# Kernel optimization log

Measured on AMD Instinct MI355X. Metric: run time of the kernel, lower is better.

The kernel has to match this reference:

```python
import jax, jax.numpy as jnp
from jax import lax
import numpy as np

N, K, L, H, LAT = 2048, 8, 64, 512, 128
NHPN, NNUC = 4, 5

def setup_inputs() -> dict:
    key = jax.random.key(0)
    ks = jax.random.split(key, 16)
    def w(k, shape):
        return (jax.random.normal(k, shape, jnp.float32) / jnp.sqrt(shape[-1])).astype(jnp.float32)
    return {
        'hpn_idx': jax.random.randint(ks[0], (N,), 0, NHPN),
        'nuc_idx': jax.random.randint(ks[1], (N, L), 0, NNUC),
        'h_nei': jax.random.normal(ks[2], (N, K, H), jnp.float32),
        'graph_latent': jax.random.normal(ks[3], (N, LAT), jnp.float32),
        'Wz_mp': w(ks[4], (H, H + NHPN)), 'bz_mp': jnp.zeros((H,), jnp.float32),
        'Wr_mp': w(ks[5], (H, NHPN)), 'br_mp': jnp.zeros((H,), jnp.float32),
        'Ur_mp': w(ks[6], (H, H)),
        'Wh_mp': w(ks[7], (H, H + NHPN)), 'bh_mp': jnp.zeros((H,), jnp.float32),
        'Wz_nuc': w(ks[8], (H, H + NNUC)), 'bz_nuc': jnp.zeros((H,), jnp.float32),
        'Wr_nuc': w(ks[9], (H, H + NNUC)), 'br_nuc': jnp.zeros((H,), jnp.float32),
        'Wh_nuc': w(ks[10], (H, H + NNUC)), 'bh_nuc': jnp.zeros((H,), jnp.float32),
        'W_hpn_nl': w(ks[11], (H, H)), 'b_hpn_nl': jnp.zeros((H,), jnp.float32),
        'W_hpn': w(ks[12], (NHPN, H)), 'b_hpn': jnp.zeros((NHPN,), jnp.float32),
        'W_nuc_nl': w(ks[13], (H, H + LAT)), 'b_nuc_nl': jnp.zeros((H,), jnp.float32),
        'W_nuc': w(ks[14], (NNUC, H)), 'b_nuc': jnp.zeros((NNUC,), jnp.float32),
        'W_topo_nl': w(ks[15], (H, H)), 'b_topo_nl': jnp.zeros((H,), jnp.float32),
        'W_topo': w(jax.random.fold_in(key, 99), (1, H)), 'b_topo': jnp.zeros((1,), jnp.float32),
    }

def _graph_gru(x, h_nei, Wz, bz, Wr, br, Ur, Wh, bh):
    # x: [N, 4] hpn one-hot; h_nei: [N, K, H] padded incoming messages
    sum_h = h_nei.sum(axis=1)
    z = jax.nn.sigmoid(jnp.concatenate([x, sum_h], axis=1) @ Wz.T + bz)
    r = jax.nn.sigmoid((x @ Wr.T + br)[:, None, :] + jnp.einsum('nkh,oh->nko', h_nei, Ur))
    sum_gated = (r * h_nei).sum(axis=1)
    pre_h = jnp.tanh(jnp.concatenate([x, sum_gated], axis=1) @ Wh.T + bh)
    return (1.0 - z) * sum_h + z * pre_h

def reference(hpn_idx, nuc_idx, h_nei, graph_latent, Wz_mp, bz_mp, Wr_mp, br_mp, Ur_mp, Wh_mp, bh_mp,
              Wz_nuc, bz_nuc, Wr_nuc, br_nuc, Wh_nuc, bh_nuc,
              W_hpn_nl, b_hpn_nl, W_hpn, b_hpn, W_nuc_nl, b_nuc_nl, W_nuc, b_nuc,
              W_topo_nl, b_topo_nl, W_topo, b_topo):
    dt = h_nei.dtype
    hpn_oh = jax.nn.one_hot(hpn_idx, NHPN, dtype=dt)
    # GraphGRU message aggregation
    msg = _graph_gru(hpn_oh, h_nei, Wz_mp, bz_mp, Wr_mp, br_mp, Ur_mp, Wh_mp, bh_mp)  # [N, H]
    # teacher-forced per-nucleotide GRU
    seq = jax.nn.one_hot(nuc_idx, NNUC, dtype=dt)  # [N, L, 5]
    def step(h, xt):
        zi = jnp.concatenate([xt, h], axis=1)
        z = jax.nn.sigmoid(zi @ Wz_nuc.T + bz_nuc)
        r = jax.nn.sigmoid(zi @ Wr_nuc.T + br_nuc)
        hi = jnp.concatenate([xt, r * h], axis=1)
        pre = jnp.tanh(hi @ Wh_nuc.T + bh_nuc)
        nh = (1.0 - z) * h + z * pre
        return nh, nh
    new_h, hs = lax.scan(step, msg, jnp.swapaxes(seq, 0, 1))  # hs: [L, N, H]
    hs = jnp.swapaxes(hs, 0, 1)  # [N, L, H]
    # nuc head: cat([hidden, graph_latent]) -> relu -> logits, without materializing the concat
    hid_part = jnp.einsum('nlh,oh->nlo', hs, W_nuc_nl[:, :H])
    lat_part = graph_latent @ W_nuc_nl[:, H:].T  # [N, H]
    nuc_hidden = jax.nn.relu(hid_part + lat_part[:, None, :] + b_nuc_nl)
    nuc_logits = jnp.einsum('nlh,oh->nlo', nuc_hidden, W_nuc) + b_nuc  # [N, L, 5]
    # hpn head on new message hidden
    hpn_logits = jax.nn.relu(new_h @ W_hpn_nl.T + b_hpn_nl) @ W_hpn.T + b_hpn  # [N, 4]
    # stop/topology head on GraphGRU output
    stop_logits = jax.nn.relu(msg @ W_topo_nl.T + b_topo_nl) @ W_topo.T + b_topo  # [N, 1]
    return jnp.concatenate([new_h.ravel(), hpn_logits.ravel(), nuc_logits.ravel(), stop_logits.ravel()])
```

## Files before the change

kernel.cpp:

```cpp
#include <hip/hip_runtime.h>
#include <math.h>

#define NROWS 2048
#define KNEI  8
#define LSEQ  64
#define HD    512
#define HD4   128
#define LATD  128
#define NHPN  4
#define NNUC  5

typedef __attribute__((ext_vector_type(8))) short s8b;
typedef __attribute__((ext_vector_type(4))) short s4b;
typedef __attribute__((ext_vector_type(4))) float f4;

#define MFMA16(a,b,c) __builtin_amdgcn_mfma_f32_16x16x32_bf16(a,b,c,0,0,0)

__device__ __forceinline__ f4 f4zero(){ f4 z; z[0]=0.f; z[1]=0.f; z[2]=0.f; z[3]=0.f; return z; }
__device__ __forceinline__ float sigf(float x){ return __fdividef(1.0f, 1.0f + __expf(-x)); }
__device__ __forceinline__ float tanhf_fast(float x){
  float e = __expf(-2.0f*fabsf(x));
  float t = __fdividef(1.0f - e, 1.0f + e);
  return x >= 0.f ? t : -t;
}
__device__ __forceinline__ unsigned short f2bf(float x){
  union{float f; unsigned u;} v; v.f = x;
  unsigned r = (v.u + 0x7FFFu + ((v.u>>16)&1u)) >> 16;
  return (unsigned short)r;
}
__device__ __forceinline__ void add4(float4& a, float4 b){ a.x+=b.x; a.y+=b.y; a.z+=b.z; a.w+=b.w; }

__device__ __forceinline__ void dma16(const short* g, const short* l){
  __builtin_amdgcn_global_load_lds(
      (const __attribute__((address_space(1))) void*)(unsigned long long)g,
      (__attribute__((address_space(3))) void*)(unsigned long long)l,
      16, 0, 0);
}


__global__ void transpose_w(const float* __restrict__ src, float* __restrict__ dst,
                            int src_cols, int col_off, int nh){
  int idx = blockIdx.x*256 + threadIdx.x;
  if (idx >= nh*HD) return;
  int h = idx / HD, o = idx - h*HD;
  dst[idx] = src[o*src_cols + col_off + h];
}

__global__ void fragprep_k(const float* __restrict__ W, short* __restrict__ dst,
                           int src_cols, int col_off){
  int idx = blockIdx.x*256 + threadIdx.x;
  if (idx >= HD*HD) return;
  int j = idx&7, l = (idx>>3)&63, tile = idx>>9;
  int kc = tile&15, ot = tile>>4;
  int row = ot*16 + (l&15), k = kc*32 + (l>>4)*8 + j;
  dst[idx] = (short)f2bf(W[(size_t)row*src_cols + col_off + k]);
}

__global__ void wxbprep2_k(const float* __restrict__ W, const float* __restrict__ b,
                           float* __restrict__ dst, int src_cols, int nc){
  int idx = blockIdx.x*256 + threadIdx.x;
  if (idx >= nc*HD) return;
  int c = idx/HD, n = idx - c*HD;
  dst[idx] = W[(size_t)n*src_cols + c] + b[n];
}

__global__ __launch_bounds__(512) void latp_k(const float* __restrict__ gl, const float* __restrict__ wtlat,
                     const float* __restrict__ bnl, float* __restrict__ latp){
  __shared__ float gls[16][LATD];
  int b = blockIdx.x, t = threadIdx.x;
  for (int i=t;i<16*LATD;i+=512) gls[i/LATD][i%LATD] = gl[(size_t)(b*16)*LATD + i];
  __syncthreads();
  float acc[16];
  float bv = bnl[t];
  #pragma unroll
  for (int r=0;r<16;++r) acc[r]=bv;
  for (int q=0;q<LATD;++q){
    float wv = wtlat[(size_t)q*HD + t];
    #pragma unroll
    for (int r=0;r<16;++r) acc[r] = fmaf(gls[r][q], wv, acc[r]);
  }
  #pragma unroll
  for (int r=0;r<16;++r) latp[(size_t)(b*16+r)*HD + t] = acc[r];
}

__global__ void sumcast_k(const float* __restrict__ h_nei,
                          float* __restrict__ sumhF, short* __restrict__ sumhB){
  int idx = blockIdx.x*512 + threadIdx.x;
  int n = idx >> 7, c4 = idx & 127;
  const float4* hn4 = (const float4*)h_nei;
  size_t base = (size_t)n*KNEI*HD4 + c4;
  float4 s = hn4[base];
  #pragma unroll
  for (int k=1;k<KNEI;++k) add4(s, hn4[base + (size_t)k*HD4]);
  ((float4*)sumhF)[(size_t)n*HD4 + c4] = s;
  s4b p;
  p[0]=(short)f2bf(s.x); p[1]=(short)f2bf(s.y); p[2]=(short)f2bf(s.z); p[3]=(short)f2bf(s.w);
  ((s4b*)sumhB)[(size_t)n*HD4 + c4] = p;
}

__global__ __launch_bounds__(512) void ggru_gemm_k(
    int mode,
    const short* __restrict__ frag,
    const short* __restrict__ A,
    const int* __restrict__ hpn_idx,
    const float* __restrict__ bias_tab,
    const float* __restrict__ sumhF, const float* __restrict__ zF_in,
    const float* __restrict__ w_topo,
    float* __restrict__ zF_out,
    float* __restrict__ hF, short* __restrict__ hB,
    float* __restrict__ topo_p)
{
  __shared__ __align__(16) short stage[16][4096];
  __shared__ int codes_s[32];
  const int tt = threadIdx.x, l = tt&63, w = tt>>6, lm = l&15, g = l>>4;
  const int rt = blockIdx.x, row0 = rt*32, cg = blockIdx.y;
  if (tt<32) codes_s[tt] = hpn_idx[row0+tt];
  const int mt = w>>2, ntp = w&3;
  const short* gsrc = frag + ((size_t)(cg*8 + w)*16)*512 + (size_t)l*8;
  #pragma unroll
  for (int kc=0;kc<8;++kc) dma16(gsrc + (size_t)kc*512, &stage[kc][w*512 + l*8]);
  s8b af[16];
  {
    const s8b* arow = (const s8b*)(A + (size_t)(row0 + mt*16 + lm)*HD);
    #pragma unroll
    for (int kc=0;kc<16;++kc) af[kc] = arow[kc*4 + g];
  }
  asm volatile("s_waitcnt vmcnt(0)" ::: "memory");
  __syncthreads();
  #pragma unroll
  for (int kc=8;kc<16;++kc) dma16(gsrc + (size_t)kc*512, &stage[kc][w*512 + l*8]);
  f4 acc[2]; acc[0]=f4zero(); acc[1]=f4zero();
  #pragma unroll
  for (int kc=0;kc<8;++kc){
    #pragma unroll
    for (int i2=0;i2<2;++i2){
      s8b b = ((const s8b*)&stage[kc][(ntp*2+i2)*512])[l];
      acc[i2] = MFMA16(af[kc], b, acc[i2]);
    }
  }
  asm volatile("s_waitcnt vmcnt(0)" ::: "memory");
  __syncthreads();
  #pragma unroll
  for (int kc=8;kc<16;++kc){
    #pragma unroll
    for (int i2=0;i2<2;++i2){
      s8b b = ((const s8b*)&stage[kc][(ntp*2+i2)*512])[l];
      acc[i2] = MFMA16(af[kc], b, acc[i2]);
    }
  }
  if (mode==0){
    #pragma unroll
    for (int i2=0;i2<2;++i2){
      const int col = cg*128 + (ntp*2+i2)*16 + lm;
      #pragma unroll
      for (int q=0;q<4;++q){
        const int r = mt*16 + g*4 + q;
        zF_out[(size_t)(row0+r)*HD + col] = sigf(acc[i2][q] + bias_tab[codes_s[r]*HD + col]);
      }
    }
  } else if (mode==1){
    #pragma unroll
    for (int i2=0;i2<2;++i2){
      const int col = cg*128 + (ntp*2+i2)*16 + lm;
      #pragma unroll
      for (int q=0;q<4;++q){
        const int r = mt*16 + g*4 + q;
        const size_t idx = (size_t)(row0+r)*HD + col;
        float pre = tanhf_fast(acc[i2][q] + bias_tab[codes_s[r]*HD + col]);
        float zv = zF_in[idx];
        float m = (1.f - zv)*sumhF[idx] + zv*pre;
        hF[idx] = m;
        hB[idx] = (short)f2bf(m);
      }
    }
  } else {
    float p[4];
    #pragma unroll
    for (int q=0;q<4;++q) p[q]=0.f;
    #pragma unroll
    for (int i2=0;i2<2;++i2){
      const int col = cg*128 + (ntp*2+i2)*16 + lm;
      float wv = w_topo[col];
      float bnl = bias_tab[col];
      #pragma unroll
      for (int q=0;q<4;++q){
        float hid = fmaxf(acc[i2][q] + bnl, 0.f);
        p[q] = fmaf(hid, wv, p[q]);
      }
    }
    #pragma unroll
    for (int s=1;s<16;s<<=1)
      #pragma unroll
      for (int q=0;q<4;++q) p[q] += __shfl_xor(p[q], s);
    if (lm==0){
      #pragma unroll
      for (int q=0;q<4;++q)
        topo_p[(size_t)(cg*4+ntp)*NROWS + row0 + mt*16 + g*4 + q] = p[q];
    }
  }
}

__global__ __launch_bounds__(512) void ggru_r_k(
    const short* __restrict__ fUr,
    const float* __restrict__ h_nei,
    const int* __restrict__ hpn_idx,
    const float* __restrict__ wxbr_mp,
    short* __restrict__ sgB)
{
  __shared__ __align__(16) short stage[16][4096];
  __shared__ float gat[32][128];
  __shared__ int codes_s[32];
  const int tt = threadIdx.x, l = tt&63, w = tt>>6, lm = l&15, g = l>>4;
  const int rt = blockIdx.x, row0 = rt*32, cg = blockIdx.y;
  if (tt<32) codes_s[tt] = hpn_idx[(row0+tt)>>3];
  const int mt = w>>2, ntp = w&3;
  const short* gsrc = fUr + ((size_t)(cg*8 + w)*16)*512 + (size_t)l*8;
  #pragma unroll
  for (int kc=0;kc<8;++kc) dma16(gsrc + (size_t)kc*512, &stage[kc][w*512 + l*8]);
  s8b af[16];
  {
    const float* hrow = h_nei + (size_t)(row0 + mt*16 + lm)*HD;
    #pragma unroll
    for (int kc=0;kc<16;++kc){
      float4 v0 = *(const float4*)&hrow[kc*32 + g*8];
      float4 v1 = *(const float4*)&hrow[kc*32 + g*8 + 4];
      s8b a;
      a[0]=(short)f2bf(v0.x); a[1]=(short)f2bf(v0.y); a[2]=(short)f2bf(v0.z); a[3]=(short)f2bf(v0.w);
      a[4]=(short)f2bf(v1.x); a[5]=(short)f2bf(v1.y); a[6]=(short)f2bf(v1.z); a[7]=(short)f2bf(v1.w);
      af[kc] = a;
    }
  }
  asm volatile("s_waitcnt vmcnt(0)" ::: "memory");
  __syncthreads();
  #pragma unroll
  for (int kc=8;kc<16;++kc) dma16(gsrc + (size_t)kc*512, &stage[kc][w*512 + l*8]);
  f4 acc[2]; acc[0]=f4zero(); acc[1]=f4zero();
  #pragma unroll
  for (int kc=0;kc<8;++kc){
    #pragma unroll
    for (int i2=0;i2<2;++i2){
      s8b b = ((const s8b*)&stage[kc][(ntp*2+i2)*512])[l];
      acc[i2] = MFMA16(af[kc], b, acc[i2]);
    }
  }
  asm volatile("s_waitcnt vmcnt(0)" ::: "memory");
  __syncthreads();
  #pragma unroll
  for (int kc=8;kc<16;++kc){
    #pragma unroll
    for (int i2=0;i2<2;++i2){
      s8b b = ((const s8b*)&stage[kc][(ntp*2+i2)*512])[l];
      acc[i2] = MFMA16(af[kc], b, acc[i2]);
    }
  }
  #pragma unroll
  for (int i2=0;i2<2;++i2){
    const int lc = (ntp*2+i2)*16 + lm;
    const int col = cg*128 + lc;
    #pragma unroll
    for (int q=0;q<4;++q){
      const int r = mt*16 + g*4 + q;
      float rv = sigf(acc[i2][q] + wxbr_mp[codes_s[r]*HD + col]);
      gat[r][lc] = rv * h_nei[(size_t)(row0+r)*HD + col];
    }
  }
  __syncthreads();
  {
    int j = tt >> 7, c = tt & 127;
    float s = 0.f;
    #pragma unroll
    for (int k=0;k<8;++k) s += gat[j*8+k][c];
    sgB[(size_t)(rt*4 + j)*HD + cg*128 + c] = (short)f2bf(s);
  }
}

__global__ __launch_bounds__(512) void zrnuc_k(
    int t, const int* __restrict__ nuc_idx,
    const short* __restrict__ fz, const short* __restrict__ fr, const short* __restrict__ fnuc,
    const short* __restrict__ hB, const float* __restrict__ hF,
    const float* __restrict__ wxbz, const float* __restrict__ wxbr,
    const float* __restrict__ latp, const float* __restrict__ w_nuc,
    float* __restrict__ zF, short* __restrict__ ghB, float* __restrict__ nucp)
{
  const int cg = blockIdx.y;
  const int mat = cg>>2;
  if (t==0 && mat==2) return;
  __shared__ __align__(16) short stage[16][4096];
  __shared__ int codes_s[64];
  const int tt = threadIdx.x, l = tt&63, w = tt>>6, lm = l&15, g = l>>4;
  const int rt = blockIdx.x, row0 = rt*64;
  const short* frag = (mat==0)?fz:((mat==1)?fr:fnuc);
  const int otb = (cg&3)*8;
  if (tt<64) codes_s[tt] = nuc_idx[(size_t)(row0+tt)*LSEQ + t];
  const int mt = w>>1, nh2 = w&1;
  const short* gsrc = frag + ((size_t)(otb + w)*16)*512 + (size_t)l*8;
  #pragma unroll
  for (int kc=0;kc<8;++kc) dma16(gsrc + (size_t)kc*512, &stage[kc][w*512 + l*8]);
  s8b af[16];
  {
    const s8b* hrow = (const s8b*)(hB + (size_t)(row0 + mt*16 + lm)*HD);
    #pragma unroll
    for (int kc=0;kc<16;++kc) af[kc] = hrow[kc*4 + g];
  }
  asm volatile("s_waitcnt vmcnt(0)" ::: "memory");
  __syncthreads();
  #pragma unroll
  for (int kc=8;kc<16;++kc) dma16(gsrc + (size_t)kc*512, &stage[kc][w*512 + l*8]);
  f4 acc[4];
  #pragma unroll
  for (int i=0;i<4;++i) acc[i]=f4zero();
  #pragma unroll
  for (int kc=0;kc<8;++kc){
    #pragma unroll
    for (int i=0;i<4;++i){
      s8b b = ((const s8b*)&stage[kc][(nh2*4+i)*512])[l];
      acc[i] = MFMA16(af[kc], b, acc[i]);
    }
  }
  asm volatile("s_waitcnt vmcnt(0)" ::: "memory");
  __syncthreads();
  #pragma unroll
  for (int kc=8;kc<16;++kc){
    #pragma unroll
    for (int i=0;i<4;++i){
      s8b b = ((const s8b*)&stage[kc][(nh2*4+i)*512])[l];
      acc[i] = MFMA16(af[kc], b, acc[i]);
    }
  }
  const int colb = (cg&3)*128;
  if (mat==0){
    #pragma unroll
    for (int i=0;i<4;++i){
      const int col = colb + (nh2*4+i)*16 + lm;
      #pragma unroll
      for (int q=0;q<4;++q){
        const int r = mt*16 + g*4 + q;
        float zv = sigf(acc[i][q] + wxbz[codes_s[r]*HD + col]);
        zF[(size_t)(row0+r)*HD + col] = zv;
      }
    }
  } else if (mat==1){
    #pragma unroll
    for (int i=0;i<4;++i){
      const int col = colb + (nh2*4+i)*16 + lm;
      #pragma unroll
      for (int q=0;q<4;++q){
        const int r = mt*16 + g*4 + q;
        float rv = sigf(acc[i][q] + wxbr[codes_s[r]*HD + col]);
        ghB[(size_t)(row0+r)*HD + col] = (short)f2bf(rv * hF[(size_t)(row0+r)*HD + col]);
      }
    }
  } else {
    float p[4][NNUC];
    #pragma unroll
    for (int q=0;q<4;++q)
      #pragma unroll
      for (int j=0;j<NNUC;++j) p[q][j]=0.f;
    #pragma unroll
    for (int i=0;i<4;++i){
      const int col = colb + (nh2*4+i)*16 + lm;
      #pragma unroll
      for (int q=0;q<4;++q){
        const int r = mt*16 + g*4 + q;
        float hid = fmaxf(acc[i][q] + latp[(size_t)(row0+r)*HD + col], 0.f);
        #pragma unroll
        for (int j=0;j<NNUC;++j) p[q][j] = fmaf(hid, w_nuc[(size_t)j*HD + col], p[q][j]);
      }
    }
    #pragma unroll
    for (int s=1;s<16;s<<=1)
      #pragma unroll
      for (int q=0;q<4;++q)
        #pragma unroll
        for (int j=0;j<NNUC;++j) p[q][j] += __shfl_xor(p[q][j], s);
    if (lm==0){
      const int slab = (cg&3)*2 + nh2;
      #pragma unroll
      for (int q=0;q<4;++q){
        const int row = row0 + mt*16 + g*4 + q;
        #pragma unroll
        for (int j=0;j<NNUC;++j)
          nucp[((size_t)slab*NROWS + row)*NNUC + j] = p[q][j];
      }
    }
  }
}

__global__ __launch_bounds__(512) void cand_k(
    int t, const int* __restrict__ nuc_idx,
    const short* __restrict__ fh,
    const short* __restrict__ ghB,
    const float* __restrict__ wxbh,
    const float* __restrict__ zF, float* __restrict__ hF, short* __restrict__ hB,
    const float* __restrict__ nucp, const float* __restrict__ b_nuc,
    float* __restrict__ out_nuc)
{
  __shared__ __align__(16) short stage[16][4096];
  __shared__ int codes_s[32];
  const int tt = threadIdx.x, l = tt&63, w = tt>>6, lm = l&15, g = l>>4;
  const int rt = blockIdx.x, row0 = rt*32, cg = blockIdx.y;
  if (tt<32) codes_s[tt] = nuc_idx[(size_t)(row0+tt)*LSEQ + t];
  const int mt = w>>2, ntp = w&3;
  const short* gsrc = fh + ((size_t)(cg*8 + w)*16)*512 + (size_t)l*8;
  #pragma unroll
  for (int kc=0;kc<8;++kc) dma16(gsrc + (size_t)kc*512, &stage[kc][w*512 + l*8]);
  s8b af[16];
  {
    const s8b* grow = (const s8b*)(ghB + (size_t)(row0 + mt*16 + lm)*HD);
    #pragma unroll
    for (int kc=0;kc<16;++kc) af[kc] = grow[kc*4 + g];
  }
  asm volatile("s_waitcnt vmcnt(0)" ::: "memory");
  __syncthreads();
  #pragma unroll
  for (int kc=8;kc<16;++kc) dma16(gsrc + (size_t)kc*512, &stage[kc][w*512 + l*8]);
  f4 acc[2]; acc[0]=f4zero(); acc[1]=f4zero();
  #pragma unroll
  for (int kc=0;kc<8;++kc){
    #pragma unroll
    for (int i2=0;i2<2;++i2){
      s8b b = ((const s8b*)&stage[kc][(ntp*2+i2)*512])[l];
      acc[i2] = MFMA16(af[kc], b, acc[i2]);
    }
  }
  asm volatile("s_waitcnt vmcnt(0)" ::: "memory");
  __syncthreads();
  #pragma unroll
  for (int kc=8;kc<16;++kc){
    #pragma unroll
    for (int i2=0;i2<2;++i2){
      s8b b = ((const s8b*)&stage[kc][(ntp*2+i2)*512])[l];
      acc[i2] = MFMA16(af[kc], b, acc[i2]);
    }
  }
  #pragma unroll
  for (int i2=0;i2<2;++i2){
    const int col = cg*128 + (ntp*2+i2)*16 + lm;
    #pragma unroll
    for (int q=0;q<4;++q){
      const int r = mt*16 + g*4 + q;
      const size_t idx = (size_t)(row0+r)*HD + col;
      float pre = tanhf_fast(acc[i2][q] + wxbh[codes_s[r]*HD + col]);
      float zv = zF[idx];
      float hn = (1.f - zv)*hF[idx] + zv*pre;
      hF[idx] = hn;
      hB[idx] = (short)f2bf(hn);
    }
  }
  if (t > 0 && cg == 0 && tt < 32*NNUC){
    int rr = tt/NNUC, j = tt - rr*NNUC;
    int row = row0 + rr;
    float s2 = b_nuc[j];
    #pragma unroll
    for (int s8=0;s8<8;++s8) s2 += nucp[((size_t)s8*NROWS + row)*NNUC + j];
    out_nuc[((size_t)row*LSEQ + (t-1))*NNUC + j] = s2;
  }
}

__global__ __launch_bounds__(512) void heads_k(
    const short* __restrict__ fnuc, const short* __restrict__ fhpn,
    const short* __restrict__ hB,
    const float* __restrict__ latp, const float* __restrict__ w_nuc,
    const float* __restrict__ b_hpn_nl, const float* __restrict__ w_hpn,
    float* __restrict__ nucpH, float* __restrict__ hpnp)
{
  __shared__ __align__(16) short stage[16][4096];
  const int tt = threadIdx.x, l = tt&63, w = tt>>6, lm = l&15, g = l>>4;
  const int rt = blockIdx.x, row0 = rt*32, cg = blockIdx.y;
  const int mat = cg>>2;
  const short* frag = mat ? fhpn : fnuc;
  const int mt = w>>2, ntp = w&3;
  const short* gsrc = frag + ((size_t)((cg&3)*8 + w)*16)*512 + (size_t)l*8;
  #pragma unroll
  for (int kc=0;kc<8;++kc) dma16(gsrc + (size_t)kc*512, &stage[kc][w*512 + l*8]);
  s8b af[16];
  {
    const s8b* hrow = (const s8b*)(hB + (size_t)(row0 + mt*16 + lm)*HD);
    #pragma unroll
    for (int kc=0;kc<16;++kc) af[kc] = hrow[kc*4 + g];
  }
  asm volatile("s_waitcnt vmcnt(0)" ::: "memory");
  __syncthreads();
  #pragma unroll
  for (int kc=8;kc<16;++kc) dma16(gsrc + (size_t)kc*512, &stage[kc][w*512 + l*8]);
  f4 acc[2]; acc[0]=f4zero(); acc[1]=f4zero();
  #pragma unroll
  for (int kc=0;kc<8;++kc){
    #pragma unroll
    for (int i2=0;i2<2;++i2){
      s8b b = ((const s8b*)&stage[kc][(ntp*2+i2)*512])[l];
      acc[i2] = MFMA16(af[kc], b, acc[i2]);
    }
  }
  asm volatile("s_waitcnt vmcnt(0)" ::: "memory");
  __syncthreads();
  #pragma unroll
  for (int kc=8;kc<16;++kc){
    #pragma unroll
    for (int i2=0;i2<2;++i2){
      s8b b = ((const s8b*)&stage[kc][(ntp*2+i2)*512])[l];
      acc[i2] = MFMA16(af[kc], b, acc[i2]);
    }
  }
  const int slab = (cg&3)*4 + ntp;
  if (mat==0){
    float p[4][NNUC];
    #pragma unroll
    for (int q=0;q<4;++q)
      #pragma unroll
      for (int j=0;j<NNUC;++j) p[q][j]=0.f;
    #pragma unroll
    for (int i2=0;i2<2;++i2){
      const int col = (cg&3)*128 + (ntp*2+i2)*16 + lm;
      #pragma unroll
      for (int q=0;q<4;++q){
        const int r = mt*16 + g*4 + q;
        float hid = fmaxf(acc[i2][q] + latp[(size_t)(row0+r)*HD + col], 0.f);
        #pragma unroll
        for (int j=0;j<NNUC;++j) p[q][j] = fmaf(hid, w_nuc[(size_t)j*HD + col], p[q][j]);
      }
    }
    #pragma unroll
    for (int s=1;s<16;s<<=1)
      #pragma unroll
      for (int q=0;q<4;++q)
        #pragma unroll
        for (int j=0;j<NNUC;++j) p[q][j] += __shfl_xor(p[q][j], s);
    if (lm==0){
      #pragma unroll
      for (int q=0;q<4;++q){
        const int row = row0 + mt*16 + g*4 + q;
        #pragma unroll
        for (int j=0;j<NNUC;++j)
          nucpH[((size_t)slab*NROWS + row)*NNUC + j] = p[q][j];
      }
    }
  } else {
    float p[4][NHPN];
    #pragma unroll
    for (int q=0;q<4;++q)
      #pragma unroll
      for (int j=0;j<NHPN;++j) p[q][j]=0.f;
    #pragma unroll
    for (int i2=0;i2<2;++i2){
      const int col = (cg&3)*128 + (ntp*2+i2)*16 + lm;
      float bnl = b_hpn_nl[col];
      #pragma unroll
      for (int q=0;q<4;++q){
        float hid = fmaxf(acc[i2][q] + bnl, 0.f);
        #pragma unroll
        for (int j=0;j<NHPN;++j) p[q][j] = fmaf(hid, w_hpn[(size_t)j*HD + col], p[q][j]);
      }
    }
    #pragma unroll
    for (int s=1;s<16;s<<=1)
      #pragma unroll
      for (int q=0;q<4;++q)
        #pragma unroll
        for (int j=0;j<NHPN;++j) p[q][j] += __shfl_xor(p[q][j], s);
    if (lm==0){
      #pragma unroll
      for (int q=0;q<4;++q){
        const int row = row0 + mt*16 + g*4 + q;
        #pragma unroll
        for (int j=0;j<NHPN;++j)
          hpnp[((size_t)slab*NROWS + row)*NHPN + j] = p[q][j];
      }
    }
  }
}

__global__ void final_red_k(const float* __restrict__ nucpH, const float* __restrict__ hpnp,
    const float* __restrict__ topo_p,
    const float* __restrict__ b_nuc, const float* __restrict__ b_hpn, const float* __restrict__ b_topo,
    const float* __restrict__ hF,
    float* __restrict__ out_newh, float* __restrict__ out_hpn, float* __restrict__ out_nuc,
    float* __restrict__ out_stop)
{
  int gid = blockIdx.x*256 + threadIdx.x;
  if (gid < NROWS*NNUC){
    int n = gid/NNUC, j = gid - n*NNUC;
    float s = b_nuc[j];
    #pragma unroll
    for (int s8=0;s8<16;++s8) s += nucpH[((size_t)s8*NROWS + n)*NNUC + j];
    out_nuc[((size_t)n*LSEQ + 63)*NNUC + j] = s;
  } else if (gid < NROWS*NNUC + NROWS*NHPN){
    int g2 = gid - NROWS*NNUC;
    int n = g2/NHPN, j = g2 - n*NHPN;
    float s = b_hpn[j];
    #pragma unroll
    for (int s8=0;s8<16;++s8) s += hpnp[((size_t)s8*NROWS + n)*NHPN + j];
    out_hpn[(size_t)n*NHPN + j] = s;
  } else if (gid < NROWS*NNUC + NROWS*NHPN + NROWS){
    int n = gid - (NROWS*NNUC + NROWS*NHPN);
    float s = b_topo[0];
    #pragma unroll
    for (int s16=0;s16<16;++s16) s += topo_p[(size_t)s16*NROWS + n];
    out_stop[n] = s;
  }
  const float4* src = (const float4*)hF;
  float4* dst = (float4*)out_newh;
  for (int i = gid; i < NROWS*HD/4; i += 32768) dst[i] = src[i];
}

extern "C" void kernel_launch(void* const* d_in, const int* in_sizes, int n_in,
                              void* d_out, int out_size, void* d_ws, size_t ws_size,
                              hipStream_t stream_){
  (void)in_sizes; (void)n_in; (void)out_size; (void)ws_size;
  const int*   hpn_idx      = (const int*)d_in[0];
  const int*   nuc_idx      = (const int*)d_in[1];
  const float* h_nei        = (const float*)d_in[2];
  const float* graph_latent = (const float*)d_in[3];
  const float* Wz_mp=(const float*)d_in[4];  const float* bz_mp=(const float*)d_in[5];
  const float* Wr_mp=(const float*)d_in[6];  const float* br_mp=(const float*)d_in[7];
  const float* Ur_mp=(const float*)d_in[8];
  const float* Wh_mp=(const float*)d_in[9];  const float* bh_mp=(const float*)d_in[10];
  const float* Wz_nuc=(const float*)d_in[11]; const float* bz_nuc=(const float*)d_in[12];
  const float* Wr_nuc=(const float*)d_in[13]; const float* br_nuc=(const float*)d_in[14];
  const float* Wh_nuc=(const float*)d_in[15]; const float* bh_nuc=(const float*)d_in[16];
  const float* W_hpn_nl=(const float*)d_in[17]; const float* b_hpn_nl=(const float*)d_in[18];
  const float* W_hpn=(const float*)d_in[19];  const float* b_hpn=(const float*)d_in[20];
  const float* W_nuc_nl=(const float*)d_in[21]; const float* b_nuc_nl=(const float*)d_in[22];
  const float* W_nuc=(const float*)d_in[23];  const float* b_nuc=(const float*)d_in[24];
  const float* W_topo_nl=(const float*)d_in[25]; const float* b_topo_nl=(const float*)d_in[26];
  const float* W_topo=(const float*)d_in[27]; const float* b_topo=(const float*)d_in[28];

  float* ws = (float*)d_ws;
  size_t off = 0;
  auto take = [&](size_t nfl){ float* p = ws + off; off += nfl; return p; };
  float* wt_nl_lat = take((size_t)LATD*HD);
  short* fz    = (short*)take((size_t)HD*HD/2);
  short* fr    = (short*)take((size_t)HD*HD/2);
  short* fh    = (short*)take((size_t)HD*HD/2);
  short* fnuc  = (short*)take((size_t)HD*HD/2);
  short* fhpn  = (short*)take((size_t)HD*HD/2);
  short* fWzh  = (short*)take((size_t)HD*HD/2);
  short* fUr   = (short*)take((size_t)HD*HD/2);
  short* fWhh  = (short*)take((size_t)HD*HD/2);
  short* fWtopo= (short*)take((size_t)HD*HD/2);
  float* wxbz = take((size_t)NNUC*HD);
  float* wxbr = take((size_t)NNUC*HD);
  float* wxbh = take((size_t)NNUC*HD);
  float* wxbz_mp = take((size_t)NHPN*HD);
  float* wxbr_mp = take((size_t)NHPN*HD);
  float* wxbh_mp = take((size_t)NHPN*HD);
  float* latp = take((size_t)NROWS*HD);
  float* hF   = take((size_t)NROWS*HD);
  short* hB   = (short*)take((size_t)NROWS*HD/2);
  short* ghB  = (short*)take((size_t)NROWS*HD/2);
  float* zF   = take((size_t)NROWS*HD);
  float* sumhF = take((size_t)NROWS*HD);
  short* sumhB = (short*)take((size_t)NROWS*HD/2);
  short* sgB   = (short*)take((size_t)NROWS*HD/2);
  float* nucp = take((size_t)8*NROWS*NNUC);
  float* nucpH= take((size_t)16*NROWS*NNUC);
  float* hpnp = take((size_t)16*NROWS*NHPN);
  float* topo_p = take((size_t)16*NROWS);

  float* out       = (float*)d_out;
  float* out_newh  = out;
  float* out_hpn   = out + (size_t)NROWS*HD;
  float* out_nuc   = out_hpn + (size_t)NROWS*NHPN;
  float* out_stop  = out_nuc + (size_t)NROWS*LSEQ*NNUC;

  transpose_w<<<(LATD*HD+255)/256, 256, 0, stream_>>>(W_nuc_nl, wt_nl_lat, HD+LATD, HD, LATD);

  const int FB = (HD*HD+255)/256;
  fragprep_k<<<FB,256,0,stream_>>>(Wz_nuc,   fz,    HD+NNUC, NNUC);
  fragprep_k<<<FB,256,0,stream_>>>(Wr_nuc,   fr,    HD+NNUC, NNUC);
  fragprep_k<<<FB,256,0,stream_>>>(Wh_nuc,   fh,    HD+NNUC, NNUC);
  fragprep_k<<<FB,256,0,stream_>>>(W_nuc_nl, fnuc,  HD+LATD, 0);
  fragprep_k<<<FB,256,0,stream_>>>(W_hpn_nl, fhpn,  HD,      0);
  fragprep_k<<<FB,256,0,stream_>>>(Wz_mp,    fWzh,  HD+NHPN, NHPN);
  fragprep_k<<<FB,256,0,stream_>>>(Ur_mp,    fUr,   HD,      0);
  fragprep_k<<<FB,256,0,stream_>>>(Wh_mp,    fWhh,  HD+NHPN, NHPN);
  fragprep_k<<<FB,256,0,stream_>>>(W_topo_nl,fWtopo,HD,      0);

  const int WB = (NNUC*HD+255)/256;
  wxbprep2_k<<<WB,256,0,stream_>>>(Wz_nuc, bz_nuc, wxbz, HD+NNUC, NNUC);
  wxbprep2_k<<<WB,256,0,stream_>>>(Wr_nuc, br_nuc, wxbr, HD+NNUC, NNUC);
  wxbprep2_k<<<WB,256,0,stream_>>>(Wh_nuc, bh_nuc, wxbh, HD+NNUC, NNUC);
  const int WB2 = (NHPN*HD+255)/256;
  wxbprep2_k<<<WB2,256,0,stream_>>>(Wz_mp, bz_mp, wxbz_mp, HD+NHPN, NHPN);
  wxbprep2_k<<<WB2,256,0,stream_>>>(Wr_mp, br_mp, wxbr_mp, NHPN,    NHPN);
  wxbprep2_k<<<WB2,256,0,stream_>>>(Wh_mp, bh_mp, wxbh_mp, HD+NHPN, NHPN);

  latp_k<<<NROWS/16, 512, 0, stream_>>>(graph_latent, wt_nl_lat, b_nuc_nl, latp);

  sumcast_k<<<512, 512, 0, stream_>>>(h_nei, sumhF, sumhB);
  ggru_gemm_k<<<dim3(64,4), 512, 0, stream_>>>(
      0, fWzh, sumhB, hpn_idx, wxbz_mp, nullptr, nullptr, nullptr,
      zF, nullptr, nullptr, nullptr);
  ggru_r_k<<<dim3(512,4), 512, 0, stream_>>>(fUr, h_nei, hpn_idx, wxbr_mp, sgB);
  ggru_gemm_k<<<dim3(64,4), 512, 0, stream_>>>(
      1, fWhh, sgB, hpn_idx, wxbh_mp, sumhF, zF, nullptr,
      nullptr, hF, hB, nullptr);
  ggru_gemm_k<<<dim3(64,4), 512, 0, stream_>>>(
      2, fWtopo, hB, hpn_idx, b_topo_nl, nullptr, nullptr, W_topo,
      nullptr, nullptr, nullptr, topo_p);

  for (int t = 0; t < LSEQ; ++t){
    zrnuc_k<<<dim3(32,12), 512, 0, stream_>>>(
        t, nuc_idx, fz, fr, fnuc, hB, hF,
        wxbz, wxbr, latp, W_nuc, zF, ghB, nucp);
    cand_k<<<dim3(64,4), 512, 0, stream_>>>(
        t, nuc_idx, fh, ghB, wxbh, zF, hF, hB,
        nucp, b_nuc, out_nuc);
  }

  heads_k<<<dim3(64,8), 512, 0, stream_>>>(
      fnuc, fhpn, hB, latp, W_nuc, b_hpn_nl, W_hpn, nucpH, hpnp);
  final_red_k<<<128, 256, 0, stream_>>>(
      nucpH, hpnp, topo_p, b_nuc, b_hpn, b_topo, hF,
      out_newh, out_hpn, out_nuc, out_stop);
}
```

Before: 2.132 ms.

## Enlarge per-block row tiles and precast neighbor messages to bf16

```diff
diff --git a/kernel.cpp b/kernel.cpp
--- a/kernel.cpp
+++ b/kernel.cpp
@@ -28,6 +28,9 @@
   unsigned r = (v.u + 0x7FFFu + ((v.u>>16)&1u)) >> 16;
   return (unsigned short)r;
 }
+__device__ __forceinline__ float bf2f(unsigned short u){
+  union{unsigned x; float f;} v; v.x = ((unsigned)u)<<16; return v.f;
+}
 __device__ __forceinline__ void add4(float4& a, float4 b){ a.x+=b.x; a.y+=b.y; a.z+=b.z; a.w+=b.w; }
 
 __device__ __forceinline__ void dma16(const short* g, const short* l){
@@ -84,14 +87,21 @@
 }
 
 __global__ void sumcast_k(const float* __restrict__ h_nei,
-                          float* __restrict__ sumhF, short* __restrict__ sumhB){
+                          float* __restrict__ sumhF, short* __restrict__ sumhB,
+                          short* __restrict__ hnB){
   int idx = blockIdx.x*512 + threadIdx.x;
   int n = idx >> 7, c4 = idx & 127;
   const float4* hn4 = (const float4*)h_nei;
   size_t base = (size_t)n*KNEI*HD4 + c4;
-  float4 s = hn4[base];
-  #pragma unroll
-  for (int k=1;k<KNEI;++k) add4(s, hn4[base + (size_t)k*HD4]);
+  float4 s = make_float4(0.f,0.f,0.f,0.f);
+  #pragma unroll
+  for (int k=0;k<KNEI;++k){
+    float4 v = hn4[base + (size_t)k*HD4];
+    add4(s, v);
+    s4b pb;
+    pb[0]=(short)f2bf(v.x); pb[1]=(short)f2bf(v.y); pb[2]=(short)f2bf(v.z); pb[3]=(short)f2bf(v.w);
+    ((s4b*)hnB)[(size_t)(n*KNEI + k)*HD4 + c4] = pb;
+  }
   ((float4*)sumhF)[(size_t)n*HD4 + c4] = s;
   s4b p;
   p[0]=(short)f2bf(s.x); p[1]=(short)f2bf(s.y); p[2]=(short)f2bf(s.z); p[3]=(short)f2bf(s.w);
@@ -202,45 +212,38 @@
 
 __global__ __launch_bounds__(512) void ggru_r_k(
     const short* __restrict__ fUr,
-    const float* __restrict__ h_nei,
+    const short* __restrict__ hnB,
     const int* __restrict__ hpn_idx,
     const float* __restrict__ wxbr_mp,
     short* __restrict__ sgB)
 {
   __shared__ __align__(16) short stage[16][4096];
-  __shared__ float gat[32][128];
-  __shared__ int codes_s[32];
+  __shared__ int codes_s[16];
   const int tt = threadIdx.x, l = tt&63, w = tt>>6, lm = l&15, g = l>>4;
-  const int rt = blockIdx.x, row0 = rt*32, cg = blockIdx.y;
-  if (tt<32) codes_s[tt] = hpn_idx[(row0+tt)>>3];
-  const int mt = w>>2, ntp = w&3;
+  const int row0 = blockIdx.x*128, cg = blockIdx.y;
+  if (tt<16) codes_s[tt] = hpn_idx[(row0>>3) + tt];
   const short* gsrc = fUr + ((size_t)(cg*8 + w)*16)*512 + (size_t)l*8;
   #pragma unroll
   for (int kc=0;kc<8;++kc) dma16(gsrc + (size_t)kc*512, &stage[kc][w*512 + l*8]);
   s8b af[16];
   {
-    const float* hrow = h_nei + (size_t)(row0 + mt*16 + lm)*HD;
-    #pragma unroll
-    for (int kc=0;kc<16;++kc){
-      float4 v0 = *(const float4*)&hrow[kc*32 + g*8];
-      float4 v1 = *(const float4*)&hrow[kc*32 + g*8 + 4];
-      s8b a;
-      a[0]=(short)f2bf(v0.x); a[1]=(short)f2bf(v0.y); a[2]=(short)f2bf(v0.z); a[3]=(short)f2bf(v0.w);
-      a[4]=(short)f2bf(v1.x); a[5]=(short)f2bf(v1.y); a[6]=(short)f2bf(v1.z); a[7]=(short)f2bf(v1.w);
-      af[kc] = a;
-    }
+    const s8b* arow = (const s8b*)(hnB + (size_t)(row0 + w*16 + lm)*HD);
+    #pragma unroll
+    for (int kc=0;kc<16;++kc) af[kc] = arow[kc*4 + g];
   }
   asm volatile("s_waitcnt vmcnt(0)" ::: "memory");
   __syncthreads();
   #pragma unroll
   for (int kc=8;kc<16;++kc) dma16(gsrc + (size_t)kc*512, &stage[kc][w*512 + l*8]);
-  f4 acc[2]; acc[0]=f4zero(); acc[1]=f4zero();
+  f4 acc[8];
+  #pragma unroll
+  for (int i=0;i<8;++i) acc[i]=f4zero();
   #pragma unroll
   for (int kc=0;kc<8;++kc){
     #pragma unroll
-    for (int i2=0;i2<2;++i2){
-      s8b b = ((const s8b*)&stage[kc][(ntp*2+i2)*512])[l];
-      acc[i2] = MFMA16(af[kc], b, acc[i2]);
+    for (int ot=0;ot<8;++ot){
+      s8b b = ((const s8b*)&stage[kc][ot*512])[l];
+      acc[ot] = MFMA16(af[kc], b, acc[ot]);
     }
   }
   asm volatile("s_waitcnt vmcnt(0)" ::: "memory");
@@ -248,29 +251,28 @@
   #pragma unroll
   for (int kc=8;kc<16;++kc){
     #pragma unroll
-    for (int i2=0;i2<2;++i2){
-      s8b b = ((const s8b*)&stage[kc][(ntp*2+i2)*512])[l];
-      acc[i2] = MFMA16(af[kc], b, acc[i2]);
-    }
-  }
-  #pragma unroll
-  for (int i2=0;i2<2;++i2){
-    const int lc = (ntp*2+i2)*16 + lm;
-    const int col = cg*128 + lc;
+    for (int ot=0;ot<8;++ot){
+      s8b b = ((const s8b*)&stage[kc][ot*512])[l];
+      acc[ot] = MFMA16(af[kc], b, acc[ot]);
+    }
+  }
+  const int nloc = w*2 + (g>>1);
+  const int code = codes_s[nloc];
+  #pragma unroll
+  for (int ot=0;ot<8;++ot){
+    const int col = cg*128 + ot*16 + lm;
+    float part = 0.f;
     #pragma unroll
     for (int q=0;q<4;++q){
-      const int r = mt*16 + g*4 + q;
-      float rv = sigf(acc[i2][q] + wxbr_mp[codes_s[r]*HD + col]);
-      gat[r][lc] = rv * h_nei[(size_t)(row0+r)*HD + col];
-    }
-  }
-  __syncthreads();
-  {
-    int j = tt >> 7, c = tt & 127;
-    float s = 0.f;
-    #pragma unroll
-    for (int k=0;k<8;++k) s += gat[j*8+k][c];
-    sgB[(size_t)(rt*4 + j)*HD + cg*128 + c] = (short)f2bf(s);
+      const int lr = w*16 + g*4 + q;
+      float rv = sigf(acc[ot][q] + wxbr_mp[code*HD + col]);
+      part += rv * bf2f((unsigned short)hnB[(size_t)(row0+lr)*HD + col]);
+    }
+    part += __shfl_xor(part, 16);
+    if ((g&1)==0){
+      const int node = (row0>>3) + nloc;
+      sgB[(size_t)node*HD + col] = (short)f2bf(part);
+    }
   }
 }
 
@@ -286,19 +288,18 @@
   const int mat = cg>>2;
   if (t==0 && mat==2) return;
   __shared__ __align__(16) short stage[16][4096];
-  __shared__ int codes_s[64];
+  __shared__ int codes_s[128];
   const int tt = threadIdx.x, l = tt&63, w = tt>>6, lm = l&15, g = l>>4;
-  const int rt = blockIdx.x, row0 = rt*64;
+  const int row0 = blockIdx.x*128;
   const short* frag = (mat==0)?fz:((mat==1)?fr:fnuc);
   const int otb = (cg&3)*8;
-  if (tt<64) codes_s[tt] = nuc_idx[(size_t)(row0+tt)*LSEQ + t];
-  const int mt = w>>1, nh2 = w&1;
+  if (tt<128) codes_s[tt] = nuc_idx[(size_t)(row0+tt)*LSEQ + t];
   const short* gsrc = frag + ((size_t)(otb + w)*16)*512 + (size_t)l*8;
   #pragma unroll
   for (int kc=0;kc<8;++kc) dma16(gsrc + (size_t)kc*512, &stage[kc][w*512 + l*8]);
   s8b af[16];
   {
-    const s8b* hrow = (const s8b*)(hB + (size_t)(row0 + mt*16 + lm)*HD);
+    const s8b* hrow = (const s8b*)(hB + (size_t)(row0 + w*16 + lm)*HD);
     #pragma unroll
     for (int kc=0;kc<16;++kc) af[kc] = hrow[kc*4 + g];
   }
@@ -306,15 +307,15 @@
   __syncthreads();
   #pragma unroll
   for (int kc=8;kc<16;++kc) dma16(gsrc + (size_t)kc*512, &stage[kc][w*512 + l*8]);
-  f4 acc[4];
-  #pragma unroll
-  for (int i=0;i<4;++i) acc[i]=f4zero();
+  f4 acc[8];
+  #pragma unroll
+  for (int i=0;i<8;++i) acc[i]=f4zero();
   #pragma unroll
   for (int kc=0;kc<8;++kc){
     #pragma unroll
-    for (int i=0;i<4;++i){
-      s8b b = ((const s8b*)&stage[kc][(nh2*4+i)*512])[l];
-      acc[i] = MFMA16(af[kc], b, acc[i]);
+    for (int ot=0;ot<8;++ot){
+      s8b b = ((const s8b*)&stage[kc][ot*512])[l];
+      acc[ot] = MFMA16(af[kc], b, acc[ot]);
     }
   }
   asm volatile("s_waitcnt vmcnt(0)" ::: "memory");
@@ -322,31 +323,30 @@
   #pragma unroll
   for (int kc=8;kc<16;++kc){
     #pragma unroll
-    for (int i=0;i<4;++i){
-      s8b b = ((const s8b*)&stage[kc][(nh2*4+i)*512])[l];
-      acc[i] = MFMA16(af[kc], b, acc[i]);
+    for (int ot=0;ot<8;++ot){
+      s8b b = ((const s8b*)&stage[kc][ot*512])[l];
+      acc[ot] = MFMA16(af[kc], b, acc[ot]);
     }
   }
   const int colb = (cg&3)*128;
   if (mat==0){
     #pragma unroll
-    for (int i=0;i<4;++i){
-      const int col = colb + (nh2*4+i)*16 + lm;
-      #pragma unroll
-      for (int q=0;q<4;++q){
-        const int r = mt*16 + g*4 + q;
-        float zv = sigf(acc[i][q] + wxbz[codes_s[r]*HD + col]);
-        zF[(size_t)(row0+r)*HD + col] = zv;
+    for (int ot=0;ot<8;++ot){
+      const int col = colb + ot*16 + lm;
+      #pragma unroll
+      for (int q=0;q<4;++q){
+        const int r = w*16 + g*4 + q;
+        zF[(size_t)(row0+r)*HD + col] = sigf(acc[ot][q] + wxbz[codes_s[r]*HD + col]);
       }
     }
   } else if (mat==1){
     #pragma unroll
-    for (int i=0;i<4;++i){
-      const int col = colb + (nh2*4+i)*16 + lm;
-      #pragma unroll
-      for (int q=0;q<4;++q){
-        const int r = mt*16 + g*4 + q;
-        float rv = sigf(acc[i][q] + wxbr[codes_s[r]*HD + col]);
+    for (int ot=0;ot<8;++ot){
+      const int col = colb + ot*16 + lm;
+      #pragma unroll
+      for (int q=0;q<4;++q){
+        const int r = w*16 + g*4 + q;
+        float rv = sigf(acc[ot][q] + wxbr[codes_s[r]*HD + col]);
         ghB[(size_t)(row0+r)*HD + col] = (short)f2bf(rv * hF[(size_t)(row0+r)*HD + col]);
       }
     }
@@ -357,12 +357,12 @@
       #pragma unroll
       for (int j=0;j<NNUC;++j) p[q][j]=0.f;
     #pragma unroll
-    for (int i=0;i<4;++i){
-      const int col = colb + (nh2*4+i)*16 + lm;
-      #pragma unroll
-      for (int q=0;q<4;++q){
-        const int r = mt*16 + g*4 + q;
-        float hid = fmaxf(acc[i][q] + latp[(size_t)(row0+r)*HD + col], 0.f);
+    for (int ot=0;ot<8;++ot){
+      const int col = colb + ot*16 + lm;
+      #pragma unroll
+      for (int q=0;q<4;++q){
+        const int r = w*16 + g*4 + q;
+        float hid = fmaxf(acc[ot][q] + latp[(size_t)(row0+r)*HD + col], 0.f);
         #pragma unroll
         for (int j=0;j<NNUC;++j) p[q][j] = fmaf(hid, w_nuc[(size_t)j*HD + col], p[q][j]);
       }
@@ -374,10 +374,10 @@
         #pragma unroll
         for (int j=0;j<NNUC;++j) p[q][j] += __shfl_xor(p[q][j], s);
     if (lm==0){
-      const int slab = (cg&3)*2 + nh2;
-      #pragma unroll
-      for (int q=0;q<4;++q){
-        const int row = row0 + mt*16 + g*4 + q;
+      const int slab = cg&3;
+      #pragma unroll
+      for (int q=0;q<4;++q){
+        const int row = row0 + w*16 + g*4 + q;
         #pragma unroll
         for (int j=0;j<NNUC;++j)
           nucp[((size_t)slab*NROWS + row)*NNUC + j] = p[q][j];
@@ -396,11 +396,11 @@
     float* __restrict__ out_nuc)
 {
   __shared__ __align__(16) short stage[16][4096];
-  __shared__ int codes_s[32];
+  __shared__ int codes_s[64];
   const int tt = threadIdx.x, l = tt&63, w = tt>>6, lm = l&15, g = l>>4;
-  const int rt = blockIdx.x, row0 = rt*32, cg = blockIdx.y;
-  if (tt<32) codes_s[tt] = nuc_idx[(size_t)(row0+tt)*LSEQ + t];
-  const int mt = w>>2, ntp = w&3;
+  const int row0 = blockIdx.x*64, cg = blockIdx.y;
+  if (tt<64) codes_s[tt] = nuc_idx[(size_t)(row0+tt)*LSEQ + t];
+  const int mt = w>>1, oth = w&1;
   const short* gsrc = fh + ((size_t)(cg*8 + w)*16)*512 + (size_t)l*8;
   #pragma unroll
   for (int kc=0;kc<8;++kc) dma16(gsrc + (size_t)kc*512, &stage[kc][w*512 + l*8]);
@@ -414,13 +414,15 @@
   __syncthreads();
   #pragma unroll
   for (int kc=8;kc<16;++kc) dma16(gsrc + (size_t)kc*512, &stage[kc][w*512 + l*8]);
-  f4 acc[2]; acc[0]=f4zero(); acc[1]=f4zero();
+  f4 acc[4];
+  #pragma unroll
+  for (int i=0;i<4;++i) acc[i]=f4zero();
   #pragma unroll
   for (int kc=0;kc<8;++kc){
     #pragma unroll
-    for (int i2=0;i2<2;++i2){
-      s8b b = ((const s8b*)&stage[kc][(ntp*2+i2)*512])[l];
-      acc[i2] = MFMA16(af[kc], b, acc[i2]);
+    for (int i=0;i<4;++i){
+      s8b b = ((const s8b*)&stage[kc][(oth*4+i)*512])[l];
+      acc[i] = MFMA16(af[kc], b, acc[i]);
     }
   }
   asm volatile("s_waitcnt vmcnt(0)" ::: "memory");
@@ -428,31 +430,31 @@
   #pragma unroll
   for (int kc=8;kc<16;++kc){
     #pragma unroll
-    for (int i2=0;i2<2;++i2){
-      s8b b = ((const s8b*)&stage[kc][(ntp*2+i2)*512])[l];
-      acc[i2] = MFMA16(af[kc], b, acc[i2]);
-    }
-  }
-  #pragma unroll
-  for (int i2=0;i2<2;++i2){
-    const int col = cg*128 + (ntp*2+i2)*16 + lm;
+    for (int i=0;i<4;++i){
+      s8b b = ((const s8b*)&stage[kc][(oth*4+i)*512])[l];
+      acc[i] = MFMA16(af[kc], b, acc[i]);
+    }
+  }
+  #pragma unroll
+  for (int i=0;i<4;++i){
+    const int col = cg*128 + (oth*4+i)*16 + lm;
     #pragma unroll
     for (int q=0;q<4;++q){
       const int r = mt*16 + g*4 + q;
       const size_t idx = (size_t)(row0+r)*HD + col;
-      float pre = tanhf_fast(acc[i2][q] + wxbh[codes_s[r]*HD + col]);
+      float pre = tanhf_fast(acc[i][q] + wxbh[codes_s[r]*HD + col]);
       float zv = zF[idx];
       float hn = (1.f - zv)*hF[idx] + zv*pre;
       hF[idx] = hn;
       hB[idx] = (short)f2bf(hn);
     }
   }
-  if (t > 0 && cg == 0 && tt < 32*NNUC){
+  if (t > 0 && cg == 0 && tt < 64*NNUC){
     int rr = tt/NNUC, j = tt - rr*NNUC;
     int row = row0 + rr;
     float s2 = b_nuc[j];
     #pragma unroll
-    for (int s8=0;s8<8;++s8) s2 += nucp[((size_t)s8*NROWS + row)*NNUC + j];
+    for (int s4=0;s4<4;++s4) s2 += nucp[((size_t)s4*NROWS + row)*NNUC + j];
     out_nuc[((size_t)row*LSEQ + (t-1))*NNUC + j] = s2;
   }
 }
@@ -652,7 +654,8 @@
   float* sumhF = take((size_t)NROWS*HD);
   short* sumhB = (short*)take((size_t)NROWS*HD/2);
   short* sgB   = (short*)take((size_t)NROWS*HD/2);
-  float* nucp = take((size_t)8*NROWS*NNUC);
+  short* hnB   = (short*)take((size_t)NROWS*KNEI*HD/2);
+  float* nucp = take((size_t)4*NROWS*NNUC);
   float* nucpH= take((size_t)16*NROWS*NNUC);
   float* hpnp = take((size_t)16*NROWS*NHPN);
   float* topo_p = take((size_t)16*NROWS);
@@ -687,11 +690,11 @@
 
   latp_k<<<NROWS/16, 512, 0, stream_>>>(graph_latent, wt_nl_lat, b_nuc_nl, latp);
 
-  sumcast_k<<<512, 512, 0, stream_>>>(h_nei, sumhF, sumhB);
+  sumcast_k<<<512, 512, 0, stream_>>>(h_nei, sumhF, sumhB, hnB);
   ggru_gemm_k<<<dim3(64,4), 512, 0, stream_>>>(
       0, fWzh, sumhB, hpn_idx, wxbz_mp, nullptr, nullptr, nullptr,
       zF, nullptr, nullptr, nullptr);
-  ggru_r_k<<<dim3(512,4), 512, 0, stream_>>>(fUr, h_nei, hpn_idx, wxbr_mp, sgB);
+  ggru_r_k<<<dim3(128,4), 512, 0, stream_>>>(fUr, hnB, hpn_idx, wxbr_mp, sgB);
   ggru_gemm_k<<<dim3(64,4), 512, 0, stream_>>>(
       1, fWhh, sgB, hpn_idx, wxbh_mp, sumhF, zF, nullptr,
       nullptr, hF, hB, nullptr);
@@ -700,10 +703,10 @@
       nullptr, nullptr, nullptr, topo_p);
 
   for (int t = 0; t < LSEQ; ++t){
-    zrnuc_k<<<dim3(32,12), 512, 0, stream_>>>(
+    zrnuc_k<<<dim3(16,12), 512, 0, stream_>>>(
         t, nuc_idx, fz, fr, fnuc, hB, hF,
         wxbz, wxbr, latp, W_nuc, zF, ghB, nucp);
-    cand_k<<<dim3(64,4), 512, 0, stream_>>>(
+    cand_k<<<dim3(32,4), 512, 0, stream_>>>(
         t, nuc_idx, fh, ghB, wxbh, zF, hF, hB,
         nucp, b_nuc, out_nuc);
   }
```

Measured after the change: 1.851 ms. 1.15x faster.
